# Kernel optimization log

Measured on AMD Instinct MI355X. Metric: run time of the kernel, lower is better.

The kernel has to match this reference:

```python
import jax, jax.numpy as jnp
import numpy as np

B, T, F2, F1 = 64, 300, 2944, 1472
RED, H, K, LN = 256, 32, 15, 7          # reduced_size, hidden_size, att_frams, layer_num
CA_RED = 320
N_CROP = T - 2 * (K - 1)                # 272 frames after the two k=15 convs
PYR = [2 ** j for j in range(1, LN)]    # [2,4,8,16,32,64]


def _pool_matrix(N, sizes):
    """Stacked AdaptiveAvgPool1d matrices: rows average torch-style bins."""
    mats = []
    for m in sizes:
        P = np.zeros((m, N), np.float32)
        for i in range(m):
            s = (i * N) // m
            e = -((-(i + 1) * N) // m)  # ceil((i+1)*N/m)
            P[i, s:e] = 1.0 / (e - s)
        mats.append(P)
    return jnp.asarray(np.concatenate(mats, 0))  # [sum(sizes), N]


def setup_inputs() -> dict:
    key = jax.random.key(0)
    ks = jax.random.split(key, 24)
    g = lambda k, sh, s=0.05: (jax.random.normal(k, sh) * s).astype(jnp.float32)
    inp = {
        "input": jax.random.normal(ks[0], (B, T, F2), jnp.float32),
        "input_length": jnp.full((B,), T, jnp.int64),
        "mean_var": g(ks[1], (F1,), 1.0),
        "std_var": jax.random.uniform(ks[2], (F1,), jnp.float32, 0.5, 1.5),
        "mean_mean": g(ks[3], (F1,), 1.0),
        "std_mean": jax.random.uniform(ks[4], (F1,), jnp.float32, 0.5, 1.5),
        # ChannelAttention params
        "ca_fc1_w": g(ks[5], (CA_RED, F2)), "ca_fc1_b": g(ks[6], (CA_RED,)),
        "ca_fc2_w": g(ks[7], (F2, CA_RED)), "ca_fc2_b": g(ks[8], (F2,)),
        # ANN (n_ANNlayers=1 -> only fc0 used)
        "ann_w": g(ks[9], (RED, F1)), "ann_b": g(ks[10], (RED,)),
        # GRU (torch gate order r,z,n)
        "gru_w_ih": g(ks[11], (3 * H, RED)), "gru_w_hh": g(ks[12], (3 * H, H)),
        "gru_b_ih": g(ks[13], (3 * H,)), "gru_b_hh": g(ks[14], (3 * H,)),
        # frame-quality head
        "q_w": g(ks[15], (1, H)), "q_b": g(ks[16], (1,)),
        # temporal attention convs
        "att_w1": g(ks[17], (1, H, K)), "att_b1": g(ks[18], (1,)),
        "att_w2": g(ks[19], (1, 1, K)), "att_b2": g(ks[20], (1,)),
        "qreg2_w": g(ks[21], (1, 2 ** LN - 1)), "qreg2_b": g(ks[22], (1,)),
    }
    return inp


def _gru(x, w_ih, w_hh, b_ih, b_hh):
    xg = jnp.einsum("btf,gf->btg", x, w_ih) + b_ih  # [B,T,3H]

    def step(h, xt):
        hg = h @ w_hh.T + b_hh
        xr, xz, xn = jnp.split(xt, 3, -1)
        hr, hz, hn = jnp.split(hg, 3, -1)
        r = jax.nn.sigmoid(xr + hr)
        z = jax.nn.sigmoid(xz + hz)
        n = jnp.tanh(xn + r * hn)
        h = (1.0 - z) * n + z * h
        return h, h

    h0 = jnp.zeros((x.shape[0], H), x.dtype)
    _, hs = jax.lax.scan(step, h0, jnp.swapaxes(xg, 0, 1))
    return jnp.swapaxes(hs, 0, 1)  # [B,T,H]


def reference(input, input_length, mean_var, std_var, mean_mean, std_mean,
              ca_fc1_w, ca_fc1_b, ca_fc2_w, ca_fc2_b, ann_w, ann_b,
              gru_w_ih, gru_w_hh, gru_b_ih, gru_b_hh, q_w, q_b,
              att_w1, att_b1, att_w2, att_b2, qreg2_w, qreg2_b):
    # --- ChannelAttention: normalize var/mean halves, sigmoid gate, fuse to 1472-d
    x_var = (input[..., :F1] - mean_var) / std_var
    x_mean = (input[..., F1:] - mean_mean) / std_mean
    xn = jnp.concatenate([x_var, x_mean], -1)                      # [B,T,2944]
    w = jax.nn.sigmoid(jnp.maximum(xn @ ca_fc1_w.T + ca_fc1_b, 0.0) @ ca_fc2_w.T + ca_fc2_b)
    feat = w[..., :F1] * x_var + w[..., F1:] * x_mean              # [B,T,1472]

    # --- ANN (single layer) + GRU
    feat = feat @ ann_w.T + ann_b                                  # [B,T,256]
    outs = _gru(feat, gru_w_ih, gru_w_hh, gru_b_ih, gru_b_hh)      # [B,T,32]

    # --- temporal attention: Conv1d(H,1,15) -> ReLU -> Conv1d(1,1,15) -> tanh
    xc = jnp.swapaxes(outs, 1, 2)                                  # [B,H,T]
    dn = ("NCH", "OIH", "NCH")
    a = jax.lax.conv_general_dilated(xc, att_w1, (1,), "VALID", dimension_numbers=dn) + att_b1[None, :, None]
    a = jnp.maximum(a, 0.0)
    a = jax.lax.conv_general_dilated(a, att_w2, (1,), "VALID", dimension_numbers=dn) + att_b2[None, :, None]
    att = jnp.tanh(a[:, 0, :])                                     # [B,N_CROP]

    q_fet = att[..., None] * outs[:, K - 1: T - (K - 1), :]        # [B,N_CROP,H]

    # --- pyramid pooling: row0 = plain mean, rest = attention-weighted means
    P = _pool_matrix(N_CROP, PYR)                                  # [126, N_CROP]
    row0 = q_fet.mean(1, keepdims=True)                            # [B,1,H]
    num = jnp.einsum("mn,bnh->bmh", P, q_fet)                      # [B,126,H]
    den = jnp.einsum("mn,bn->bm", P, att)[..., None]               # [B,126,1]
    q_pool = jnp.concatenate([row0, num / den], 1)                 # [B,127,H]

    q_each = (q_pool @ q_w.T + q_b)[..., 0]                        # [B,127]
    score = q_each @ qreg2_w.T + qreg2_b                           # [B,1]
    return score
```

## Files before the change

### kernel.cpp

```cpp
#include <hip/hip_runtime.h>


typedef unsigned short u16t;
typedef unsigned int   u32t;
typedef float  f32x4 __attribute__((ext_vector_type(4)));
typedef u32t   u32x4 __attribute__((ext_vector_type(4)));
typedef __bf16 bf16x8 __attribute__((ext_vector_type(8)));

__device__ __forceinline__ f32x4 mfma_b(u32x4 a, u32x4 b, f32x4 c){
  return __builtin_amdgcn_mfma_f32_16x16x32_bf16(
      __builtin_bit_cast(bf16x8, a), __builtin_bit_cast(bf16x8, b), c, 0, 0, 0);
}

#define GLDS16(SRC, DST)                                                    \
  __builtin_amdgcn_global_load_lds(                                         \
      (const __attribute__((address_space(1))) void*)(SRC),                 \
      (__attribute__((address_space(3))) void*)(DST), 16, 0, 0)

__device__ __forceinline__ void split3(float x, u16t& h, u16t& m, u16t& l){
  u32t u = __float_as_uint(x);
  h = (u16t)(u >> 16);
  float d1 = x - __uint_as_float(u & 0xFFFF0000u);
  u32t u1 = __float_as_uint(d1);
  m = (u16t)(u1 >> 16);
  float d2 = d1 - __uint_as_float(u1 & 0xFFFF0000u);
  l = (u16t)(__float_as_uint(d2) >> 16);
}

__device__ __forceinline__ u32t resid(u32t u){
  float d = __uint_as_float(u) - __uint_as_float(u & 0xFFFF0000u);
  return __float_as_uint(d);
}

__device__ __forceinline__ void split8_3(u32x4 a, u32x4 b,
                                         u32x4& H, u32x4& M, u32x4& L){
  u32t r1[8], r2[8];
#pragma unroll
  for (int j = 0; j < 4; j++){ r1[j] = resid(a[j]); r1[4 + j] = resid(b[j]); }
#pragma unroll
  for (int j = 0; j < 8; j++){ r2[j] = resid(r1[j]); }
  H[0] = __builtin_amdgcn_perm(a[1], a[0], 0x07060302u);
  H[1] = __builtin_amdgcn_perm(a[3], a[2], 0x07060302u);
  H[2] = __builtin_amdgcn_perm(b[1], b[0], 0x07060302u);
  H[3] = __builtin_amdgcn_perm(b[3], b[2], 0x07060302u);
  M[0] = __builtin_amdgcn_perm(r1[1], r1[0], 0x07060302u);
  M[1] = __builtin_amdgcn_perm(r1[3], r1[2], 0x07060302u);
  M[2] = __builtin_amdgcn_perm(r1[5], r1[4], 0x07060302u);
  M[3] = __builtin_amdgcn_perm(r1[7], r1[6], 0x07060302u);
  L[0] = __builtin_amdgcn_perm(r2[1], r2[0], 0x07060302u);
  L[1] = __builtin_amdgcn_perm(r2[3], r2[2], 0x07060302u);
  L[2] = __builtin_amdgcn_perm(r2[5], r2[4], 0x07060302u);
  L[3] = __builtin_amdgcn_perm(r2[7], r2[6], 0x07060302u);
}

__device__ __forceinline__ void mfma6(const u32x4& AH, const u32x4& AM, const u32x4& AL,
                                      const u32x4& BH, const u32x4& BM, const u32x4& BL,
                                      f32x4& acc){
  acc = mfma_b(AL, BH, acc);
  acc = mfma_b(AM, BM, acc);
  acc = mfma_b(AH, BL, acc);
  acc = mfma_b(AM, BH, acc);
  acc = mfma_b(AH, BM, acc);
  acc = mfma_b(AH, BH, acc);
}

__global__ __launch_bounds__(256) void prep_params_kernel(
    const float* __restrict__ mv, const float* __restrict__ sv,
    const float* __restrict__ mm, const float* __restrict__ sm,
    double* __restrict__ mu, double* __restrict__ rinv){
  int f = blockIdx.x * 256 + threadIdx.x;
  if (f < 2944){
    if (f < 1472){ mu[f] = (double)mv[f]; rinv[f] = 1.0 / (double)sv[f]; }
    else         { mu[f] = (double)mm[f - 1472]; rinv[f] = 1.0 / (double)sm[f - 1472]; }
  }
}

__global__ __launch_bounds__(256) void split3_w1_kernel(
    const float* __restrict__ w, const double* __restrict__ rinv,
    u16t* __restrict__ wh, u16t* __restrict__ wm, u16t* __restrict__ wl){
  int id = blockIdx.x * 256 + threadIdx.x;
  if (id < 320 * 2944){
    float v = (float)((double)w[id] * rinv[id % 2944]);
    split3(v, wh[id], wm[id], wl[id]);
  }
}

__global__ __launch_bounds__(256) void split3_plain_kernel(
    const float* __restrict__ w, u16t* __restrict__ wh, u16t* __restrict__ wm,
    u16t* __restrict__ wl, int n){
  int id = blockIdx.x * 256 + threadIdx.x;
  if (id < n) split3(w[id], wh[id], wm[id], wl[id]);
}

__global__ __launch_bounds__(64) void b1p_kernel(
    const float* __restrict__ w1, const float* __restrict__ b1,
    const double* __restrict__ mu, const double* __restrict__ rinv,
    float* __restrict__ b1p){
  int n = blockIdx.x, lane = threadIdx.x;
  double s = 0.0;
  for (int k = lane; k < 2944; k += 64)
    s += (double)w1[n * 2944 + k] * rinv[k] * mu[k];
#pragma unroll
  for (int o = 32; o > 0; o >>= 1) s += __shfl_xor(s, o);
  if (lane == 0) b1p[n] = (float)((double)b1[n] - s);
}

__global__ __launch_bounds__(256) void make_wc_kernel(
    const float* __restrict__ wih, const float* __restrict__ annw,
    const float* __restrict__ annb, const float* __restrict__ bih,
    u16t* __restrict__ wch, u16t* __restrict__ wcm, u16t* __restrict__ wcl,
    float* __restrict__ bc){
  int id = blockIdx.x * 256 + threadIdx.x;
  if (id < 96 * 1472){
    int g = id / 1472, k = id - g * 1472;
    double s = 0.0;
    for (int r = 0; r < 256; r++)
      s += (double)wih[g * 256 + r] * (double)annw[r * 1472 + k];
    split3((float)s, wch[id], wcm[id], wcl[id]);
  } else if (id < 96 * 1472 + 96){
    int g = id - 96 * 1472;
    double s = (double)bih[g];
    for (int r = 0; r < 256; r++)
      s += (double)wih[g * 256 + r] * (double)annb[r];
    bc[g] = (float)s;
  }
}

__global__ __launch_bounds__(512) void gemm1_kernel(
    const float* __restrict__ x,
    const u16t* __restrict__ w1h, const u16t* __restrict__ w1m,
    const u16t* __restrict__ w1l, const float* __restrict__ b1p,
    u16t* __restrict__ h1h, u16t* __restrict__ h1m, u16t* __restrict__ h1l){
  __shared__ float lA[64 * 32];
  __shared__ u16t lBh[160 * 32], lBm[160 * 32], lBl[160 * 32];
  const int tid = threadIdx.x, wave = tid >> 6, lane = tid & 63;
  const int wm = wave >> 1, wn = wave & 1;
  const int bid = blockIdx.x;
  const int xcd = bid & 7, j = bid >> 3;
  const int n0 = (xcd & 4) ? 160 : 0;
  const int m0 = ((xcd & 3) * 75 + j) * 64;
  const int ar = lane >> 3, as = lane & 7;
  const int br = lane >> 2, bs = lane & 3;
  const int g = lane >> 4, r15 = lane & 15;
  f32x4 acc[5] = {};
  for (int k0 = 0; k0 < 2944; k0 += 32){
    __syncthreads();
    {
      int i = wave;
      int row = i * 8 + ar;
      GLDS16(x + (size_t)(m0 + row) * 2944 + k0 + ((as ^ (row & 7)) << 2), lA + (i << 8));
    }
    for (int i = wave; i < 10; i += 8){
      int row = i * 16 + br;
      size_t src = (size_t)(n0 + row) * 2944 + k0 + ((bs ^ ((row >> 1) & 3)) << 3);
      uint4 vh = *(const uint4*)(w1h + src);
      uint4 vm = *(const uint4*)(w1m + src);
      uint4 vl = *(const uint4*)(w1l + src);
      int d = (i << 9) + (lane << 3);
      *(uint4*)(lBh + d) = vh;
      *(uint4*)(lBm + d) = vm;
      *(uint4*)(lBl + d) = vl;
    }
    __syncthreads();
    u32x4 AH, AM, AL;
    {
      int row = wm * 16 + r15;
      const char* base = (const char*)lA + (row << 7);
      u32x4 a0 = *(const u32x4*)(base + ((((g << 1) + 0) ^ (row & 7)) << 4));
      u32x4 a1 = *(const u32x4*)(base + ((((g << 1) + 1) ^ (row & 7)) << 4));
      split8_3(a0, a1, AH, AM, AL);
    }
#pragma unroll
    for (int fn = 0; fn < 5; fn++){
      int row = wn * 80 + fn * 16 + r15;
      int off = (row << 6) + ((g ^ ((row >> 1) & 3)) << 4);
      u32x4 BH = *(const u32x4*)((const char*)lBh + off);
      u32x4 BM = *(const u32x4*)((const char*)lBm + off);
      u32x4 BL = *(const u32x4*)((const char*)lBl + off);
      mfma6(AH, AM, AL, BH, BM, BL, acc[fn]);
    }
  }
#pragma unroll
  for (int fn = 0; fn < 5; fn++){
    int col = n0 + wn * 80 + fn * 16 + r15;
    float bias = b1p[col];
    int mb = m0 + wm * 16 + ((lane >> 4) << 2);
#pragma unroll
    for (int r = 0; r < 4; r++){
      float v = fmaxf(acc[fn][r] + bias, 0.f);
      size_t o = (size_t)(mb + r) * 320 + col;
      split3(v, h1h[o], h1m[o], h1l[o]);
    }
  }
}

__global__ __launch_bounds__(512) void gemm2_kernel(
    const u16t* __restrict__ h1h, const u16t* __restrict__ h1m,
    const u16t* __restrict__ h1l,
    const u16t* __restrict__ w2h, const u16t* __restrict__ w2m,
    const u16t* __restrict__ w2l, const float* __restrict__ b2,
    const float* __restrict__ x, const double* __restrict__ mu,
    const double* __restrict__ rinv,
    u16t* __restrict__ feath, u16t* __restrict__ featm, u16t* __restrict__ featl){
  __shared__ u16t lAh[192 * 32], lAm[192 * 32], lAl[192 * 32];
  __shared__ u16t lBh[128 * 32], lBm[128 * 32], lBl[128 * 32];
  const int tid = threadIdx.x, wave = tid >> 6, lane = tid & 63;
  const int wm = wave >> 1, wn = wave & 1;
  const int bid = blockIdx.x;
  const int work = (bid & 7) * 288 + (bid >> 3);
  if (work >= 2300) return;
  const int mg = work / 23, f0i = work - mg * 23;
  const int m0 = mg * 192, f0 = f0i * 64;
  const int br = lane >> 2, bs = lane & 3;
  const int g = lane >> 4, r15 = lane & 15;
  f32x4 acc[3][4] = {};
  for (int k0 = 0; k0 < 320; k0 += 32){
    __syncthreads();
    for (int i = wave; i < 12; i += 8){
      int row = i * 16 + br;
      int cs = (bs ^ ((row >> 1) & 3)) << 3;
      size_t sa = (size_t)(m0 + row) * 320 + k0 + cs;
      uint4 vh = *(const uint4*)(h1h + sa);
      uint4 vm = *(const uint4*)(h1m + sa);
      uint4 vl = *(const uint4*)(h1l + sa);
      int d = (i << 9) + (lane << 3);
      *(uint4*)(lAh + d) = vh;
      *(uint4*)(lAm + d) = vm;
      *(uint4*)(lAl + d) = vl;
    }
    {
      int i = wave;
      int row = i * 16 + br;
      int cs = (bs ^ ((row >> 1) & 3)) << 3;
      int w2row = (((row >> 4) & 1) * 1472) + f0 + ((row >> 5) << 4) + (row & 15);
      size_t sb = (size_t)w2row * 320 + k0 + cs;
      GLDS16(w2h + sb, lBh + (i << 9));
      GLDS16(w2m + sb, lBm + (i << 9));
      GLDS16(w2l + sb, lBl + (i << 9));
    }
    __syncthreads();
    u32x4 AH[3], AM[3], AL[3];
#pragma unroll
    for (int fm = 0; fm < 3; fm++){
      int row = wm * 48 + fm * 16 + r15;
      int off = (row << 6) + ((g ^ ((row >> 1) & 3)) << 4);
      AH[fm] = *(const u32x4*)((const char*)lAh + off);
      AM[fm] = *(const u32x4*)((const char*)lAm + off);
      AL[fm] = *(const u32x4*)((const char*)lAl + off);
    }
#pragma unroll
    for (int fn = 0; fn < 4; fn++){
      int row = wn * 64 + fn * 16 + r15;
      int off = (row << 6) + ((g ^ ((row >> 1) & 3)) << 4);
      u32x4 BH = *(const u32x4*)((const char*)lBh + off);
      u32x4 BM = *(const u32x4*)((const char*)lBm + off);
      u32x4 BL = *(const u32x4*)((const char*)lBl + off);
#pragma unroll
      for (int fm = 0; fm < 3; fm++)
        mfma6(AH[fm], AM[fm], AL[fm], BH, BM, BL, acc[fm][fn]);
    }
  }
#pragma unroll
  for (int cg = 0; cg < 2; cg++){
    int f = f0 + wn * 32 + cg * 16 + r15;
    float blo = b2[f], bhi = b2[1472 + f];
    double muv = mu[f], riv = rinv[f];
    double mum = mu[1472 + f], rim = rinv[1472 + f];
#pragma unroll
    for (int fm = 0; fm < 3; fm++){
      int mb = m0 + wm * 48 + fm * 16 + ((lane >> 4) << 2);
#pragma unroll
      for (int r = 0; r < 4; r++){
        int m = mb + r;
        float zl = acc[fm][2 * cg][r] + blo;
        float zh = acc[fm][2 * cg + 1][r] + bhi;
        float wl = 1.f / (1.f + expf(-zl));
        float wh = 1.f / (1.f + expf(-zh));
        float xv = (float)(((double)x[(size_t)m * 2944 + f] - muv) * riv);
        float xm = (float)(((double)x[(size_t)m * 2944 + 1472 + f] - mum) * rim);
        float fv = wl * xv + wh * xm;
        size_t o = (size_t)m * 1472 + f;
        split3(fv, feath[o], featm[o], featl[o]);
      }
    }
  }
}

__global__ __launch_bounds__(256) void gemm3_kernel(
    const u16t* __restrict__ feath, const u16t* __restrict__ featm,
    const u16t* __restrict__ featl,
    const u16t* __restrict__ wch, const u16t* __restrict__ wcm,
    const u16t* __restrict__ wcl, const float* __restrict__ bc,
    float* __restrict__ xg){
  __shared__ u16t lAh[32 * 32], lAm[32 * 32], lAl[32 * 32];
  __shared__ u16t lBh[96 * 32], lBm[96 * 32], lBl[96 * 32];
  const int tid = threadIdx.x, wave = tid >> 6, lane = tid & 63;
  const int wm = wave >> 1, wn = wave & 1;
  const int bid = blockIdx.x;
  const int m0 = ((bid & 7) * 75 + (bid >> 3)) * 32;
  const int br = lane >> 2, bs = lane & 3;
  const int g = lane >> 4, r15 = lane & 15;
  f32x4 acc[3] = {};
  for (int k0 = 0; k0 < 1472; k0 += 32){
    __syncthreads();
    for (int i = wave; i < 2; i += 4){
      int row = i * 16 + br;
      int cs = (bs ^ ((row >> 1) & 3)) << 3;
      size_t sa = (size_t)(m0 + row) * 1472 + k0 + cs;
      GLDS16(feath + sa, lAh + (i << 9));
      GLDS16(featm + sa, lAm + (i << 9));
      GLDS16(featl + sa, lAl + (i << 9));
    }
    for (int i = wave; i < 6; i += 4){
      int row = i * 16 + br;
      int cs = (bs ^ ((row >> 1) & 3)) << 3;
      size_t sb = (size_t)row * 1472 + k0 + cs;
      uint4 vh = *(const uint4*)(wch + sb);
      uint4 vm = *(const uint4*)(wcm + sb);
      uint4 vl = *(const uint4*)(wcl + sb);
      int d = (i << 9) + (lane << 3);
      *(uint4*)(lBh + d) = vh;
      *(uint4*)(lBm + d) = vm;
      *(uint4*)(lBl + d) = vl;
    }
    __syncthreads();
    u32x4 AH, AM, AL;
    {
      int row = wm * 16 + r15;
      int off = (row << 6) + ((g ^ ((row >> 1) & 3)) << 4);
      AH = *(const u32x4*)((const char*)lAh + off);
      AM = *(const u32x4*)((const char*)lAm + off);
      AL = *(const u32x4*)((const char*)lAl + off);
    }
#pragma unroll
    for (int fn = 0; fn < 3; fn++){
      int row = wn * 48 + fn * 16 + r15;
      int off = (row << 6) + ((g ^ ((row >> 1) & 3)) << 4);
      u32x4 BH = *(const u32x4*)((const char*)lBh + off);
      u32x4 BM = *(const u32x4*)((const char*)lBm + off);
      u32x4 BL = *(const u32x4*)((const char*)lBl + off);
      mfma6(AH, AM, AL, BH, BM, BL, acc[fn]);
    }
  }
#pragma unroll
  for (int fn = 0; fn < 3; fn++){
    int col = wn * 48 + fn * 16 + r15;
    float bias = bc[col];
    int mb = m0 + wm * 16 + ((lane >> 4) << 2);
#pragma unroll
    for (int r = 0; r < 4; r++)
      xg[(size_t)(mb + r) * 96 + col] = acc[fn][r] + bias;
  }
}

__global__ __launch_bounds__(128) void gru_kernel(
    const float* __restrict__ xg, const float* __restrict__ whh,
    const float* __restrict__ bhh, float* __restrict__ outs){
  const int b = blockIdx.x, tid = threadIdx.x;
  __shared__ float hs[32];
  __shared__ double hg[96];
  double wr[32];
  double bias = 0.0;
  if (tid < 96){
#pragma unroll
    for (int j = 0; j < 32; j++) wr[j] = (double)whh[tid * 32 + j];
    bias = (double)bhh[tid];
  }
  if (tid < 32) hs[tid] = 0.f;
  __syncthreads();
  const float* xb = xg + (size_t)b * 300 * 96;
  float* ob = outs + (size_t)b * 300 * 32;
  for (int t = 0; t < 300; t++){
    if (tid < 96){
      double s0 = 0.0, s1 = 0.0;
#pragma unroll
      for (int j = 0; j < 16; j++){
        s0 += wr[j] * (double)hs[j];
        s1 += wr[16 + j] * (double)hs[16 + j];
      }
      hg[tid] = bias + s0 + s1;
    }
    __syncthreads();
    if (tid < 32){
      float xr  = xb[t * 96 + tid];
      float xz  = xb[t * 96 + 32 + tid];
      float xnv = xb[t * 96 + 64 + tid];
      float r = 1.f / (1.f + expf(-(float)((double)xr + hg[tid])));
      float z = 1.f / (1.f + expf(-(float)((double)xz + hg[32 + tid])));
      float n = tanhf((float)((double)xnv + (double)r * hg[64 + tid]));
      float h = (1.f - z) * n + z * hs[tid];
      hs[tid] = h;
      ob[t * 32 + tid] = h;
    }
    __syncthreads();
  }
}

__global__ __launch_bounds__(64) void attn_final_kernel(
    const float* __restrict__ outs, const float* __restrict__ w1,
    const float* __restrict__ b1, const float* __restrict__ w2,
    const float* __restrict__ b2, const float* __restrict__ qw,
    const float* __restrict__ qb, const float* __restrict__ rw,
    const float* __restrict__ rb, float* __restrict__ out){
  const int b = blockIdx.x, lane = threadIdx.x;
  __shared__ float a1[286];
  __shared__ double attv[272];
  __shared__ double sd[272];
  __shared__ float w1s[480];
  __shared__ float qws[32];
  const float* ob = outs + (size_t)b * 300 * 32;
  for (int i = lane; i < 480; i += 64) w1s[i] = w1[i];
  if (lane < 32) qws[lane] = qw[lane];
  __syncthreads();
  const double bb1 = (double)b1[0];
  for (int t = lane; t < 286; t += 64){
    double s = bb1;
    for (int k = 0; k < 15; k++){
      const float* row = ob + (t + k) * 32;
#pragma unroll
      for (int c = 0; c < 32; c++) s += (double)row[c] * (double)w1s[c * 15 + k];
    }
    a1[t] = fmaxf((float)s, 0.f);
  }
  __syncthreads();
  const double bb2 = (double)b2[0];
  for (int t = lane; t < 272; t += 64){
    double s = bb2;
#pragma unroll
    for (int k = 0; k < 15; k++) s += (double)a1[t + k] * (double)w2[k];
    double a = tanh(s);
    attv[t] = a;
    const float* row = ob + (t + 14) * 32;
    double d = 0.0;
#pragma unroll
    for (int c = 0; c < 32; c++) d += (double)row[c] * (double)qws[c];
    sd[t] = a * d;
  }
  __syncthreads();
  const double qb0 = (double)qb[0];
  double part = 0.0;
  double msum = 0.0;
  for (int t = lane; t < 272; t += 64) msum += sd[t];
  part += (double)rw[0] * (msum / 272.0);
  if (lane == 0) part += (double)rw[0] * qb0 + (double)rb[0];
  for (int j = lane; j < 126; j += 64){
    int mcur = 2, i = j;
    while (i >= mcur){ i -= mcur; mcur <<= 1; }
    int s = (i * 272) / mcur;
    int e = ((i + 1) * 272 + mcur - 1) / mcur;
    double S = 0.0, A = 0.0;
    for (int n = s; n < e; n++){ S += sd[n]; A += attv[n]; }
    part += (double)rw[1 + j] * (S / A + qb0);
  }
#pragma unroll
  for (int o = 32; o > 0; o >>= 1) part += __shfl_xor(part, o);
  if (lane == 0) out[b] = (float)part;
}

extern "C" void kernel_launch(void* const* d_in, const int* in_sizes, int n_in,
                              void* d_out, int out_size, void* d_ws, size_t ws_size,
                              hipStream_t stream){
  const float* input     = (const float*)d_in[0];
  const float* mean_var  = (const float*)d_in[2];
  const float* std_var   = (const float*)d_in[3];
  const float* mean_mean = (const float*)d_in[4];
  const float* std_mean  = (const float*)d_in[5];
  const float* ca1w = (const float*)d_in[6];
  const float* ca1b = (const float*)d_in[7];
  const float* ca2w = (const float*)d_in[8];
  const float* ca2b = (const float*)d_in[9];
  const float* annw = (const float*)d_in[10];
  const float* annb = (const float*)d_in[11];
  const float* wih  = (const float*)d_in[12];
  const float* whh  = (const float*)d_in[13];
  const float* bih  = (const float*)d_in[14];
  const float* bhh  = (const float*)d_in[15];
  const float* qw   = (const float*)d_in[16];
  const float* qb   = (const float*)d_in[17];
  const float* aw1  = (const float*)d_in[18];
  const float* ab1  = (const float*)d_in[19];
  const float* aw2  = (const float*)d_in[20];
  const float* ab2  = (const float*)d_in[21];
  const float* rw   = (const float*)d_in[22];
  const float* rb   = (const float*)d_in[23];
  float* out = (float*)d_out;

  char* ws = (char*)d_ws;
  size_t off = 0;
  auto alloc = [&](size_t bytes){
    size_t o = off; off += (bytes + 255) & ~(size_t)255; return o;
  };
  const size_t H1 = (size_t)19200 * 320, FT = (size_t)19200 * 1472;
  u16t* h1h = (u16t*)(ws + alloc(H1 * 2));
  u16t* h1m = (u16t*)(ws + alloc(H1 * 2));
  u16t* h1l = (u16t*)(ws + alloc(H1 * 2));
  u16t* feath = (u16t*)(ws + alloc(FT * 2));
  u16t* featm = (u16t*)(ws + alloc(FT * 2));
  u16t* featl = (u16t*)(ws + alloc(FT * 2));
  float* xg    = (float*)(ws + alloc((size_t)19200 * 96 * 4));
  float* outsb = (float*)(ws + alloc((size_t)19200 * 32 * 4));
  u16t* w1h = (u16t*)(ws + alloc((size_t)320 * 2944 * 2));
  u16t* w1m = (u16t*)(ws + alloc((size_t)320 * 2944 * 2));
  u16t* w1l = (u16t*)(ws + alloc((size_t)320 * 2944 * 2));
  u16t* w2h = (u16t*)(ws + alloc((size_t)2944 * 320 * 2));
  u16t* w2m = (u16t*)(ws + alloc((size_t)2944 * 320 * 2));
  u16t* w2l = (u16t*)(ws + alloc((size_t)2944 * 320 * 2));
  u16t* wch = (u16t*)(ws + alloc((size_t)96 * 1472 * 2));
  u16t* wcm = (u16t*)(ws + alloc((size_t)96 * 1472 * 2));
  u16t* wcl = (u16t*)(ws + alloc((size_t)96 * 1472 * 2));
  double* mu   = (double*)(ws + alloc(2944 * 8));
  double* rinv = (double*)(ws + alloc(2944 * 8));
  float* b1p   = (float*)(ws + alloc(320 * 4));
  float* bc    = (float*)(ws + alloc(96 * 4));
  (void)ws_size; (void)in_sizes; (void)n_in; (void)out_size;

  prep_params_kernel<<<12, 256, 0, stream>>>(mean_var, std_var, mean_mean, std_mean, mu, rinv);
  split3_w1_kernel<<<3680, 256, 0, stream>>>(ca1w, rinv, w1h, w1m, w1l);
  split3_plain_kernel<<<3680, 256, 0, stream>>>(ca2w, w2h, w2m, w2l, 2944 * 320);
  b1p_kernel<<<320, 64, 0, stream>>>(ca1w, ca1b, mu, rinv, b1p);
  make_wc_kernel<<<553, 256, 0, stream>>>(wih, annw, annb, bih, wch, wcm, wcl, bc);
  gemm1_kernel<<<600, 512, 0, stream>>>(input, w1h, w1m, w1l, b1p, h1h, h1m, h1l);
  gemm2_kernel<<<2304, 512, 0, stream>>>(h1h, h1m, h1l, w2h, w2m, w2l, ca2b,
                                         input, mu, rinv, feath, featm, featl);
  gemm3_kernel<<<600, 256, 0, stream>>>(feath, featm, featl, wch, wcm, wcl, bc, xg);
  gru_kernel<<<64, 128, 0, stream>>>(xg, whh, bhh, outsb);
  attn_final_kernel<<<64, 64, 0, stream>>>(outsb, aw1, ab1, aw2, ab2, qw, qb, rw, rb, out);
}
```

Measured before the change: 946.3 us.

## Register-prefetch next K tile in GEMM kernels instead of direct global-to-LDS loads

Replaces the global_load_lds and synchronous load-then-store staging in the three split-bf16 GEMM kernels with register prefetching. The loads for the next K tile are issued right after the current tile is written to LDS, so global latency overlaps with the MFMA work. The cost is more VGPRs for the staging registers, which may lower occupancy, and the A tiles now take an extra register hop into LDS.

```diff
diff --git a/kernel.cpp b/kernel.cpp
--- a/kernel.cpp
+++ b/kernel.cpp
@@ -11,11 +11,6 @@
   return __builtin_amdgcn_mfma_f32_16x16x32_bf16(
       __builtin_bit_cast(bf16x8, a), __builtin_bit_cast(bf16x8, b), c, 0, 0, 0);
 }
-
-#define GLDS16(SRC, DST)                                                    \
-  __builtin_amdgcn_global_load_lds(                                         \
-      (const __attribute__((address_space(1))) void*)(SRC),                 \
-      (__attribute__((address_space(3))) void*)(DST), 16, 0, 0)
 
 __device__ __forceinline__ void split3(float x, u16t& h, u16t& m, u16t& l){
   u32t u = __float_as_uint(x);
@@ -142,25 +137,42 @@
   const int ar = lane >> 3, as = lane & 7;
   const int br = lane >> 2, bs = lane & 3;
   const int g = lane >> 4, r15 = lane & 15;
+  uint4 rA, rB0h, rB0m, rB0l, rB1h, rB1m, rB1l;
+  const int aRow = wave * 8 + ar;
+  const size_t aBase = (size_t)(m0 + aRow) * 2944 + ((as ^ (aRow & 7)) << 2);
+  const int bRow0 = wave * 16 + br;
+  const size_t bBase0 = (size_t)(n0 + bRow0) * 2944 + ((bs ^ ((bRow0 >> 1) & 3)) << 3);
+  const int bRow1 = (wave + 8) * 16 + br;
+  const size_t bBase1 = (size_t)(n0 + bRow1) * 2944 + ((bs ^ ((bRow1 >> 1) & 3)) << 3);
+  auto issue = [&](int k0){
+    rA  = *(const uint4*)(x + aBase + k0);
+    rB0h = *(const uint4*)(w1h + bBase0 + k0);
+    rB0m = *(const uint4*)(w1m + bBase0 + k0);
+    rB0l = *(const uint4*)(w1l + bBase0 + k0);
+    if (wave < 2){
+      rB1h = *(const uint4*)(w1h + bBase1 + k0);
+      rB1m = *(const uint4*)(w1m + bBase1 + k0);
+      rB1l = *(const uint4*)(w1l + bBase1 + k0);
+    }
+  };
   f32x4 acc[5] = {};
+  issue(0);
   for (int k0 = 0; k0 < 2944; k0 += 32){
     __syncthreads();
+    *(uint4*)((char*)lA + (wave << 10) + (lane << 4)) = rA;
     {
-      int i = wave;
-      int row = i * 8 + ar;
-      GLDS16(x + (size_t)(m0 + row) * 2944 + k0 + ((as ^ (row & 7)) << 2), lA + (i << 8));
-    }
-    for (int i = wave; i < 10; i += 8){
-      int row = i * 16 + br;
-      size_t src = (size_t)(n0 + row) * 2944 + k0 + ((bs ^ ((row >> 1) & 3)) << 3);
-      uint4 vh = *(const uint4*)(w1h + src);
-      uint4 vm = *(const uint4*)(w1m + src);
-      uint4 vl = *(const uint4*)(w1l + src);
-      int d = (i << 9) + (lane << 3);
-      *(uint4*)(lBh + d) = vh;
-      *(uint4*)(lBm + d) = vm;
-      *(uint4*)(lBl + d) = vl;
-    }
+      int d = (wave << 10) + (lane << 4);
+      *(uint4*)((char*)lBh + d) = rB0h;
+      *(uint4*)((char*)lBm + d) = rB0m;
+      *(uint4*)((char*)lBl + d) = rB0l;
+      if (wave < 2){
+        int d1 = ((wave + 8) << 10) + (lane << 4);
+        *(uint4*)((char*)lBh + d1) = rB1h;
+        *(uint4*)((char*)lBm + d1) = rB1m;
+        *(uint4*)((char*)lBl + d1) = rB1l;
+      }
+    }
+    if (k0 + 32 < 2944) issue(k0 + 32);
     __syncthreads();
     u32x4 AH, AM, AL;
     {
@@ -213,31 +225,47 @@
   const int m0 = mg * 192, f0 = f0i * 64;
   const int br = lane >> 2, bs = lane & 3;
   const int g = lane >> 4, r15 = lane & 15;
+  uint4 rA0h, rA0m, rA0l, rA1h, rA1m, rA1l, rBh, rBm, rBl;
+  const int aRow0 = wave * 16 + br;
+  const size_t aBase0 = (size_t)(m0 + aRow0) * 320 + ((bs ^ ((aRow0 >> 1) & 3)) << 3);
+  const int aRow1 = (wave + 8) * 16 + br;
+  const size_t aBase1 = (size_t)(m0 + aRow1) * 320 + ((bs ^ ((aRow1 >> 1) & 3)) << 3);
+  const int bRow = wave * 16 + br;
+  const int w2row = (((bRow >> 4) & 1) * 1472) + f0 + ((bRow >> 5) << 4) + (bRow & 15);
+  const size_t bBase = (size_t)w2row * 320 + ((bs ^ ((bRow >> 1) & 3)) << 3);
+  auto issue = [&](int k0){
+    rA0h = *(const uint4*)(h1h + aBase0 + k0);
+    rA0m = *(const uint4*)(h1m + aBase0 + k0);
+    rA0l = *(const uint4*)(h1l + aBase0 + k0);
+    if (wave < 4){
+      rA1h = *(const uint4*)(h1h + aBase1 + k0);
+      rA1m = *(const uint4*)(h1m + aBase1 + k0);
+      rA1l = *(const uint4*)(h1l + aBase1 + k0);
+    }
+    rBh = *(const uint4*)(w2h + bBase + k0);
+    rBm = *(const uint4*)(w2m + bBase + k0);
+    rBl = *(const uint4*)(w2l + bBase + k0);
+  };
   f32x4 acc[3][4] = {};
+  issue(0);
   for (int k0 = 0; k0 < 320; k0 += 32){
     __syncthreads();
-    for (int i = wave; i < 12; i += 8){
-      int row = i * 16 + br;
-      int cs = (bs ^ ((row >> 1) & 3)) << 3;
-      size_t sa = (size_t)(m0 + row) * 320 + k0 + cs;
-      uint4 vh = *(const uint4*)(h1h + sa);
-      uint4 vm = *(const uint4*)(h1m + sa);
-      uint4 vl = *(const uint4*)(h1l + sa);
-      int d = (i << 9) + (lane << 3);
-      *(uint4*)(lAh + d) = vh;
-      *(uint4*)(lAm + d) = vm;
-      *(uint4*)(lAl + d) = vl;
-    }
     {
-      int i = wave;
-      int row = i * 16 + br;
-      int cs = (bs ^ ((row >> 1) & 3)) << 3;
-      int w2row = (((row >> 4) & 1) * 1472) + f0 + ((row >> 5) << 4) + (row & 15);
-      size_t sb = (size_t)w2row * 320 + k0 + cs;
-      GLDS16(w2h + sb, lBh + (i << 9));
-      GLDS16(w2m + sb, lBm + (i << 9));
-      GLDS16(w2l + sb, lBl + (i << 9));
-    }
+      int d = (wave << 10) + (lane << 4);
+      *(uint4*)((char*)lAh + d) = rA0h;
+      *(uint4*)((char*)lAm + d) = rA0m;
+      *(uint4*)((char*)lAl + d) = rA0l;
+      if (wave < 4){
+        int d1 = ((wave + 8) << 10) + (lane << 4);
+        *(uint4*)((char*)lAh + d1) = rA1h;
+        *(uint4*)((char*)lAm + d1) = rA1m;
+        *(uint4*)((char*)lAl + d1) = rA1l;
+      }
+      *(uint4*)((char*)lBh + d) = rBh;
+      *(uint4*)((char*)lBm + d) = rBm;
+      *(uint4*)((char*)lBl + d) = rBl;
+    }
+    if (k0 + 32 < 320) issue(k0 + 32);
     __syncthreads();
     u32x4 AH[3], AM[3], AL[3];
 #pragma unroll
@@ -300,29 +328,50 @@
   const int m0 = ((bid & 7) * 75 + (bid >> 3)) * 32;
   const int br = lane >> 2, bs = lane & 3;
   const int g = lane >> 4, r15 = lane & 15;
+  uint4 rAh, rAm, rAl, rB0h, rB0m, rB0l, rB1h, rB1m, rB1l;
+  const int aRow = wave * 16 + br;
+  const size_t aBase = (size_t)(m0 + aRow) * 1472 + ((bs ^ ((aRow >> 1) & 3)) << 3);
+  const int bRow0 = wave * 16 + br;
+  const size_t bBase0 = (size_t)bRow0 * 1472 + ((bs ^ ((bRow0 >> 1) & 3)) << 3);
+  const int bRow1 = (wave + 4) * 16 + br;
+  const size_t bBase1 = (size_t)bRow1 * 1472 + ((bs ^ ((bRow1 >> 1) & 3)) << 3);
+  auto issue = [&](int k0){
+    if (wave < 2){
+      rAh = *(const uint4*)(feath + aBase + k0);
+      rAm = *(const uint4*)(featm + aBase + k0);
+      rAl = *(const uint4*)(featl + aBase + k0);
+    }
+    rB0h = *(const uint4*)(wch + bBase0 + k0);
+    rB0m = *(const uint4*)(wcm + bBase0 + k0);
+    rB0l = *(const uint4*)(wcl + bBase0 + k0);
+    if (wave < 2){
+      rB1h = *(const uint4*)(wch + bBase1 + k0);
+      rB1m = *(const uint4*)(wcm + bBase1 + k0);
+      rB1l = *(const uint4*)(wcl + bBase1 + k0);
+    }
+  };
   f32x4 acc[3] = {};
+  issue(0);
   for (int k0 = 0; k0 < 1472; k0 += 32){
     __syncthreads();
-    for (int i = wave; i < 2; i += 4){
-      int row = i * 16 + br;
-      int cs = (bs ^ ((row >> 1) & 3)) << 3;
-      size_t sa = (size_t)(m0 + row) * 1472 + k0 + cs;
-      GLDS16(feath + sa, lAh + (i << 9));
-      GLDS16(featm + sa, lAm + (i << 9));
-      GLDS16(featl + sa, lAl + (i << 9));
-    }
-    for (int i = wave; i < 6; i += 4){
-      int row = i * 16 + br;
-      int cs = (bs ^ ((row >> 1) & 3)) << 3;
-      size_t sb = (size_t)row * 1472 + k0 + cs;
-      uint4 vh = *(const uint4*)(wch + sb);
-      uint4 vm = *(const uint4*)(wcm + sb);
-      uint4 vl = *(const uint4*)(wcl + sb);
-      int d = (i << 9) + (lane << 3);
-      *(uint4*)(lBh + d) = vh;
-      *(uint4*)(lBm + d) = vm;
-      *(uint4*)(lBl + d) = vl;
-    }
+    {
+      int d = (wave << 10) + (lane << 4);
+      if (wave < 2){
+        *(uint4*)((char*)lAh + d) = rAh;
+        *(uint4*)((char*)lAm + d) = rAm;
+        *(uint4*)((char*)lAl + d) = rAl;
+      }
+      *(uint4*)((char*)lBh + d) = rB0h;
+      *(uint4*)((char*)lBm + d) = rB0m;
+      *(uint4*)((char*)lBl + d) = rB0l;
+      if (wave < 2){
+        int d1 = ((wave + 4) << 10) + (lane << 4);
+        *(uint4*)((char*)lBh + d1) = rB1h;
+        *(uint4*)((char*)lBm + d1) = rB1m;
+        *(uint4*)((char*)lBl + d1) = rB1l;
+      }
+    }
+    if (k0 + 32 < 1472) issue(k0 + 32);
     __syncthreads();
     u32x4 AH, AM, AL;
     {
```

Result: no change. 963.8 us (+1.8%).

## Split A tile once into LDS and give each gemm1 wave two M fragments

Applied to the files above, without the earlier changes.

gemm1 now runs 4 waves per block instead of 8. Each wave computes two 16-row M fragments, so every B fragment read from LDS is reused twice. The fp32 input tile is no longer copied straight to LDS and re-split into hi/mid/lo bf16 by every wave that reads it. Each element is loaded into registers, split once, and stored as three bf16 planes with a swizzled layout. This cuts redundant split work and B LDS reads, but drops the async global-to-LDS load, doubles the accumulator registers, and halves the threads per block.

```diff
diff --git a/kernel.cpp b/kernel.cpp
--- a/kernel.cpp
+++ b/kernel.cpp
@@ -25,32 +25,6 @@
   m = (u16t)(u1 >> 16);
   float d2 = d1 - __uint_as_float(u1 & 0xFFFF0000u);
   l = (u16t)(__float_as_uint(d2) >> 16);
-}
-
-__device__ __forceinline__ u32t resid(u32t u){
-  float d = __uint_as_float(u) - __uint_as_float(u & 0xFFFF0000u);
-  return __float_as_uint(d);
-}
-
-__device__ __forceinline__ void split8_3(u32x4 a, u32x4 b,
-                                         u32x4& H, u32x4& M, u32x4& L){
-  u32t r1[8], r2[8];
-#pragma unroll
-  for (int j = 0; j < 4; j++){ r1[j] = resid(a[j]); r1[4 + j] = resid(b[j]); }
-#pragma unroll
-  for (int j = 0; j < 8; j++){ r2[j] = resid(r1[j]); }
-  H[0] = __builtin_amdgcn_perm(a[1], a[0], 0x07060302u);
-  H[1] = __builtin_amdgcn_perm(a[3], a[2], 0x07060302u);
-  H[2] = __builtin_amdgcn_perm(b[1], b[0], 0x07060302u);
-  H[3] = __builtin_amdgcn_perm(b[3], b[2], 0x07060302u);
-  M[0] = __builtin_amdgcn_perm(r1[1], r1[0], 0x07060302u);
-  M[1] = __builtin_amdgcn_perm(r1[3], r1[2], 0x07060302u);
-  M[2] = __builtin_amdgcn_perm(r1[5], r1[4], 0x07060302u);
-  M[3] = __builtin_amdgcn_perm(r1[7], r1[6], 0x07060302u);
-  L[0] = __builtin_amdgcn_perm(r2[1], r2[0], 0x07060302u);
-  L[1] = __builtin_amdgcn_perm(r2[3], r2[2], 0x07060302u);
-  L[2] = __builtin_amdgcn_perm(r2[5], r2[4], 0x07060302u);
-  L[3] = __builtin_amdgcn_perm(r2[7], r2[6], 0x07060302u);
 }
 
 __device__ __forceinline__ void mfma6(const u32x4& AH, const u32x4& AM, const u32x4& AL,
@@ -126,12 +100,12 @@
   }
 }
 
-__global__ __launch_bounds__(512) void gemm1_kernel(
+__global__ __launch_bounds__(256) void gemm1_kernel(
     const float* __restrict__ x,
     const u16t* __restrict__ w1h, const u16t* __restrict__ w1m,
     const u16t* __restrict__ w1l, const float* __restrict__ b1p,
     u16t* __restrict__ h1h, u16t* __restrict__ h1m, u16t* __restrict__ h1l){
-  __shared__ float lA[64 * 32];
+  __shared__ u16t lAh[64 * 32], lAm[64 * 32], lAl[64 * 32];
   __shared__ u16t lBh[160 * 32], lBm[160 * 32], lBl[160 * 32];
   const int tid = threadIdx.x, wave = tid >> 6, lane = tid & 63;
   const int wm = wave >> 1, wn = wave & 1;
@@ -139,18 +113,21 @@
   const int xcd = bid & 7, j = bid >> 3;
   const int n0 = (xcd & 4) ? 160 : 0;
   const int m0 = ((xcd & 3) * 75 + j) * 64;
-  const int ar = lane >> 3, as = lane & 7;
+  const int ar0 = tid >> 3, ar1 = 32 + ar0, au = tid & 7;
+  const int ak0 = (((au >> 1) ^ ((ar0 >> 1) & 3)) << 3) + ((au & 1) << 2);
+  const int ak1 = (((au >> 1) ^ ((ar1 >> 1) & 3)) << 3) + ((au & 1) << 2);
+  const size_t aSrc0 = (size_t)(m0 + ar0) * 2944 + ak0;
+  const size_t aSrc1 = (size_t)(m0 + ar1) * 2944 + ak1;
+  const int aDst0 = ar0 * 32 + au * 4;
+  const int aDst1 = ar1 * 32 + au * 4;
   const int br = lane >> 2, bs = lane & 3;
   const int g = lane >> 4, r15 = lane & 15;
-  f32x4 acc[5] = {};
+  f32x4 acc[2][5] = {};
   for (int k0 = 0; k0 < 2944; k0 += 32){
     __syncthreads();
-    {
-      int i = wave;
-      int row = i * 8 + ar;
-      GLDS16(x + (size_t)(m0 + row) * 2944 + k0 + ((as ^ (row & 7)) << 2), lA + (i << 8));
-    }
-    for (int i = wave; i < 10; i += 8){
+    float4 va0 = *(const float4*)(x + aSrc0 + k0);
+    float4 va1 = *(const float4*)(x + aSrc1 + k0);
+    for (int i = wave; i < 10; i += 4){
       int row = i * 16 + br;
       size_t src = (size_t)(n0 + row) * 2944 + k0 + ((bs ^ ((row >> 1) & 3)) << 3);
       uint4 vh = *(const uint4*)(w1h + src);
@@ -161,14 +138,39 @@
       *(uint4*)(lBm + d) = vm;
       *(uint4*)(lBl + d) = vl;
     }
-    __syncthreads();
-    u32x4 AH, AM, AL;
     {
-      int row = wm * 16 + r15;
-      const char* base = (const char*)lA + (row << 7);
-      u32x4 a0 = *(const u32x4*)(base + ((((g << 1) + 0) ^ (row & 7)) << 4));
-      u32x4 a1 = *(const u32x4*)(base + ((((g << 1) + 1) ^ (row & 7)) << 4));
-      split8_3(a0, a1, AH, AM, AL);
+      u16t h[4], m[4], l[4];
+      split3(va0.x, h[0], m[0], l[0]);
+      split3(va0.y, h[1], m[1], l[1]);
+      split3(va0.z, h[2], m[2], l[2]);
+      split3(va0.w, h[3], m[3], l[3]);
+      uint2 ph, pm, pl;
+      ph.x = (u32t)h[0] | ((u32t)h[1] << 16); ph.y = (u32t)h[2] | ((u32t)h[3] << 16);
+      pm.x = (u32t)m[0] | ((u32t)m[1] << 16); pm.y = (u32t)m[2] | ((u32t)m[3] << 16);
+      pl.x = (u32t)l[0] | ((u32t)l[1] << 16); pl.y = (u32t)l[2] | ((u32t)l[3] << 16);
+      *(uint2*)(lAh + aDst0) = ph;
+      *(uint2*)(lAm + aDst0) = pm;
+      *(uint2*)(lAl + aDst0) = pl;
+      split3(va1.x, h[0], m[0], l[0]);
+      split3(va1.y, h[1], m[1], l[1]);
+      split3(va1.z, h[2], m[2], l[2]);
+      split3(va1.w, h[3], m[3], l[3]);
+      ph.x = (u32t)h[0] | ((u32t)h[1] << 16); ph.y = (u32t)h[2] | ((u32t)h[3] << 16);
+      pm.x = (u32t)m[0] | ((u32t)m[1] << 16); pm.y = (u32t)m[2] | ((u32t)m[3] << 16);
+      pl.x = (u32t)l[0] | ((u32t)l[1] << 16); pl.y = (u32t)l[2] | ((u32t)l[3] << 16);
+      *(uint2*)(lAh + aDst1) = ph;
+      *(uint2*)(lAm + aDst1) = pm;
+      *(uint2*)(lAl + aDst1) = pl;
+    }
+    __syncthreads();
+    u32x4 AH[2], AM[2], AL[2];
+#pragma unroll
+    for (int fm = 0; fm < 2; fm++){
+      int row = wm * 32 + fm * 16 + r15;
+      int off = (row << 6) + ((g ^ ((row >> 1) & 3)) << 4);
+      AH[fm] = *(const u32x4*)((const char*)lAh + off);
+      AM[fm] = *(const u32x4*)((const char*)lAm + off);
+      AL[fm] = *(const u32x4*)((const char*)lAl + off);
     }
 #pragma unroll
     for (int fn = 0; fn < 5; fn++){
@@ -177,19 +179,24 @@
       u32x4 BH = *(const u32x4*)((const char*)lBh + off);
       u32x4 BM = *(const u32x4*)((const char*)lBm + off);
       u32x4 BL = *(const u32x4*)((const char*)lBl + off);
-      mfma6(AH, AM, AL, BH, BM, BL, acc[fn]);
+#pragma unroll
+      for (int fm = 0; fm < 2; fm++)
+        mfma6(AH[fm], AM[fm], AL[fm], BH, BM, BL, acc[fm][fn]);
     }
   }
 #pragma unroll
   for (int fn = 0; fn < 5; fn++){
-    int col = n0 + wn * 80 + fn * 16 + r15;
+    int col = n0 + wn * 80 + fn * 16 + (lane & 15);
     float bias = b1p[col];
-    int mb = m0 + wm * 16 + ((lane >> 4) << 2);
-#pragma unroll
-    for (int r = 0; r < 4; r++){
-      float v = fmaxf(acc[fn][r] + bias, 0.f);
-      size_t o = (size_t)(mb + r) * 320 + col;
-      split3(v, h1h[o], h1m[o], h1l[o]);
+#pragma unroll
+    for (int fm = 0; fm < 2; fm++){
+      int mb = m0 + wm * 32 + fm * 16 + ((lane >> 4) << 2);
+#pragma unroll
+      for (int r = 0; r < 4; r++){
+        float v = fmaxf(acc[fm][fn][r] + bias, 0.f);
+        size_t o = (size_t)(mb + r) * 320 + col;
+        split3(v, h1h[o], h1m[o], h1l[o]);
+      }
     }
   }
 }
@@ -519,7 +526,7 @@
   split3_plain_kernel<<<3680, 256, 0, stream>>>(ca2w, w2h, w2m, w2l, 2944 * 320);
   b1p_kernel<<<320, 64, 0, stream>>>(ca1w, ca1b, mu, rinv, b1p);
   make_wc_kernel<<<553, 256, 0, stream>>>(wih, annw, annb, bih, wch, wcm, wcl, bc);
-  gemm1_kernel<<<600, 512, 0, stream>>>(input, w1h, w1m, w1l, b1p, h1h, h1m, h1l);
+  gemm1_kernel<<<600, 256, 0, stream>>>(input, w1h, w1m, w1l, b1p, h1h, h1m, h1l);
   gemm2_kernel<<<2304, 512, 0, stream>>>(h1h, h1m, h1l, w2h, w2m, w2l, ca2b,
                                          input, mu, rinv, feath, featm, featl);
   gemm3_kernel<<<600, 256, 0, stream>>>(feath, featm, featl, wch, wcm, wcl, bc, xg);
```

Result: no change. 951.9 us (+0.6%).
